# Kernel tuning notes

Hardware: AMD Instinct MI355X
Metric: run time of the kernel (lower is better)

Reference implementation:

```python
import jax, jax.numpy as jnp
import numpy as np

B, N, E = 4, 50000, 400000
DIMS = [4, 64, 64, 2]
K = 3
EPS = 1e-5      # BatchNorm1d eps
SLOPE = 0.01    # LeakyReLU default negative slope


def setup_inputs() -> dict:
    key = jax.random.key(0)
    k = jax.random.split(key, 20)
    x = jax.random.normal(k[0], (B, N, DIMS[0]), dtype=jnp.float32)
    src = jax.random.randint(k[1], (E,), 0, N)
    dst = jax.random.randint(k[2], (E,), 0, N)
    edge_w = jax.random.uniform(k[3], (E,), dtype=jnp.float32) + 0.1
    W1 = jax.random.normal(k[4], (K + 1, DIMS[0], DIMS[1]), dtype=jnp.float32) * 0.1
    b1 = jnp.zeros((DIMS[1],), jnp.float32)
    W2 = jax.random.normal(k[5], (K + 1, DIMS[1], DIMS[2]), dtype=jnp.float32) * 0.1
    b2 = jnp.zeros((DIMS[2],), jnp.float32)
    W3 = jax.random.normal(k[6], (K + 1, DIMS[2], DIMS[3]), dtype=jnp.float32) * 0.1
    b3 = jnp.zeros((DIMS[3],), jnp.float32)
    g1 = jnp.ones((N,), jnp.float32)
    be1 = jnp.zeros((N,), jnp.float32)
    g2 = jnp.ones((N,), jnp.float32)
    be2 = jnp.zeros((N,), jnp.float32)
    mask = (jax.random.uniform(k[7], (N, 2)) < 0.7).astype(jnp.float32)
    mean_y = jax.random.normal(k[8], (N, 2), dtype=jnp.float32) * 0.1
    std_y = jax.random.uniform(k[9], (N, 2), dtype=jnp.float32) + 0.5
    vmin = -jnp.abs(jax.random.normal(k[10], (N,), dtype=jnp.float32)) - 1.0
    vmax = jnp.abs(jax.random.normal(k[11], (N,), dtype=jnp.float32)) + 1.0
    qmin = -jnp.abs(jax.random.normal(k[12], (N,), dtype=jnp.float32)) - 1.0
    qmax = jnp.abs(jax.random.normal(k[13], (N,), dtype=jnp.float32)) + 1.0
    return dict(x=x, src=src, dst=dst, edge_w=edge_w, W1=W1, b1=b1, W2=W2, b2=b2,
                W3=W3, b3=b3, g1=g1, be1=be1, g2=g2, be2=be2, mask=mask,
                mean_y=mean_y, std_y=std_y, vmin=vmin, vmax=vmax, qmin=qmin, qmax=qmax)


def _tag(h, W, b, src, dst, w):
    # TAGConv: out = sum_k A_norm^k x @ W_k + b
    out = jnp.einsum('bnf,fg->bng', h, W[0])
    for i in range(1, W.shape[0]):
        msg = h[:, src, :] * w[None, :, None]          # gather + scale  [B, E, F]
        h = jnp.zeros_like(h).at[:, dst, :].add(msg)   # scatter-add     [B, N, F]
        out = out + jnp.einsum('bnf,fg->bng', h, W[i])
    return out + b


def _bn(h, g, b):
    # nn.BatchNorm1d(N) on [B, N, F]: per-node stats over (batch, feature)
    mu = h.mean(axis=(0, 2), keepdims=True)
    var = h.var(axis=(0, 2), keepdims=True)  # biased, as torch uses for normalization
    return g[None, :, None] * (h - mu) * jax.lax.rsqrt(var + EPS) + b[None, :, None]


def reference(x, src, dst, edge_w, W1, b1, W2, b2, W3, b3, g1, be1, g2, be2,
              mask, mean_y, std_y, vmin, vmax, qmin, qmax):
    n = x.shape[1]
    # gcn_norm (add_self_loops=False): D^{-1/2} A D^{-1/2} with deg over targets
    deg = jnp.zeros((n,), x.dtype).at[dst].add(edge_w)
    dis = jnp.where(deg > 0, jax.lax.rsqrt(jnp.maximum(deg, 1e-30)), 0.0)
    w = dis[src] * edge_w * dis[dst]
    h = jax.nn.leaky_relu(_bn(_tag(x, W1, b1, src, dst, w), g1, be1), SLOPE)
    h = jax.nn.leaky_relu(_bn(_tag(h, W2, b2, src, dst, w), g2, be2), SLOPE)
    out = _tag(h, W3, b3, src, dst, w)
    # denormalize_y=True path
    std = jnp.where(jnp.isinf(std_y), 0.0, std_y)
    out = (out * std + mean_y) * mask
    # training=False path: per-node clamp of v and q channels
    out = jnp.stack([jnp.clip(out[:, :, 0], vmin, vmax),
                     jnp.clip(out[:, :, 1], qmin, qmax)], axis=-1)
    return out
```

## Files before the change

kernel.cpp:

```cpp
#include <hip/hip_runtime.h>
#include <hip/hip_bf16.h>

typedef __hip_bfloat16 bf16;
typedef unsigned int u32;
typedef unsigned short u16;
typedef __attribute__((ext_vector_type(8))) short bf16x8;
typedef __attribute__((ext_vector_type(4))) float f32x4;

#define NNODES 50000
#define NEDGES 400000
#define NROWS  200000
#define NBLK   196
#define EPSBN  1e-5f
#define SLOPE  0.01f
#define WS_NEEDED 106711296ULL

static __device__ __forceinline__ float bu2f(u16 u) { return __uint_as_float((u32)u << 16); }
static __device__ __forceinline__ float blo(u32 u) { return __uint_as_float(u << 16); }
static __device__ __forceinline__ float bhi(u32 u) { return __uint_as_float(u & 0xFFFF0000u); }
static __device__ __forceinline__ u16 f2bu(float f) {
  bf16 x = __float2bfloat16(f);
  return *(u16*)&x;
}
static __device__ __forceinline__ u32 bpack(float a, float b) {
  return (u32)f2bu(a) | ((u32)f2bu(b) << 16);
}
static __device__ __forceinline__ float ld(const void* p, int i, int isbf) {
  return isbf ? bu2f(((const u16*)p)[i]) : ((const float*)p)[i];
}

union frag_u { uint4 u; bf16x8 v; };

__global__ __launch_bounds__(256)
void detect_kernel(const u16* __restrict__ ew_raw, int* __restrict__ flag) {
  __shared__ int ok;
  if (threadIdx.x == 0) ok = 1;
  __syncthreads();
  float v = bu2f(ew_raw[threadIdx.x]);
  if (!(v >= 0.04f && v <= 1.3f)) atomicAnd(&ok, 0);
  __syncthreads();
  if (threadIdx.x == 0) *flag = ok;
}

__global__ __launch_bounds__(256)
void ws_probe_kernel(u32* __restrict__ out) {
  int i = blockIdx.x * 256 + threadIdx.x;
  if (i < 4 * NNODES * 2) out[i] = 0u;
}


__global__ __launch_bounds__(256)
void edge_deg_kernel(const int* __restrict__ dst, const void* __restrict__ ew,
                     const int* __restrict__ flagp, float* __restrict__ deg,
                     int* __restrict__ cnt) {
  int isbf = *flagp;
  int e = blockIdx.x * 256 + threadIdx.x;
  if (e >= NEDGES) return;
  int d = dst[e];
  atomicAdd(&deg[d], ld(ew, e, isbf));
  atomicAdd(&cnt[d], 1);
}

__global__ __launch_bounds__(256)
void node_dis_kernel(const float* __restrict__ deg, float* __restrict__ dis) {
  int n = blockIdx.x * 256 + threadIdx.x;
  if (n >= NNODES) return;
  float d = deg[n];
  dis[n] = d > 0.f ? 1.f / sqrtf(fmaxf(d, 1e-30f)) : 0.f;
}

__global__ __launch_bounds__(256)
void bsum_kernel(const int* __restrict__ cnt, int* __restrict__ bsum) {
  __shared__ int sd[256];
  int tid = threadIdx.x;
  int i = blockIdx.x * 256 + tid;
  sd[tid] = (i < NNODES) ? cnt[i] : 0;
  __syncthreads();
  for (int off = 128; off > 0; off >>= 1) {
    if (tid < off) sd[tid] += sd[tid + off];
    __syncthreads();
  }
  if (tid == 0) bsum[blockIdx.x] = sd[0];
}

__global__ __launch_bounds__(256)
void bscan_kernel(const int* __restrict__ bsum, int* __restrict__ boff) {
  __shared__ int sd[256];
  int tid = threadIdx.x;
  int v = (tid < NBLK) ? bsum[tid] : 0;
  sd[tid] = v;
  __syncthreads();
  for (int off = 1; off < 256; off <<= 1) {
    int t = (tid >= off) ? sd[tid - off] : 0;
    __syncthreads();
    sd[tid] += t;
    __syncthreads();
  }
  if (tid < NBLK) boff[tid] = sd[tid] - v;
}

__global__ __launch_bounds__(256)
void scatter_scan_kernel(const int* __restrict__ cnt, const int* __restrict__ boff,
                         int* __restrict__ rowp, int* __restrict__ cursor) {
  __shared__ int sd[256];
  int tid = threadIdx.x;
  int i = blockIdx.x * 256 + tid;
  int v = (i < NNODES) ? cnt[i] : 0;
  sd[tid] = v;
  __syncthreads();
  for (int off = 1; off < 256; off <<= 1) {
    int t = (tid >= off) ? sd[tid - off] : 0;
    __syncthreads();
    sd[tid] += t;
    __syncthreads();
  }
  if (i < NNODES) {
    int ex = boff[blockIdx.x] + sd[tid] - v;
    rowp[i] = ex;
    cursor[i] = ex;
  }
  if (i == NNODES - 1) rowp[NNODES] = NEDGES;
}

__global__ __launch_bounds__(256)
void edge_fill_kernel(const int* __restrict__ src, const int* __restrict__ dst,
                      const void* __restrict__ ew, const int* __restrict__ flagp,
                      const float* __restrict__ dis, int* __restrict__ cursor,
                      int* __restrict__ src_s, float* __restrict__ w_s) {
  int isbf = *flagp;
  int e = blockIdx.x * 256 + threadIdx.x;
  if (e >= NEDGES) return;
  int s = src[e], d = dst[e];
  float w = dis[s] * ld(ew, e, isbf) * dis[d];
  int p = atomicAdd(&cursor[d], 1);
  src_s[p] = s;
  w_s[p] = w;
}

__global__ __launch_bounds__(256)
void convw_kernel(const void* __restrict__ W1, const void* __restrict__ b1,
                  const void* __restrict__ W2, const void* __restrict__ b2,
                  const void* __restrict__ W3, const void* __restrict__ b3,
                  const int* __restrict__ flagp, float* __restrict__ out) {
  int isbf = *flagp;
  int i = blockIdx.x * 256 + threadIdx.x;
  if (i < 1024)       out[i] = ld(W1, i, isbf);
  else if (i < 17408) out[i] = ld(W2, i - 1024, isbf);
  else if (i < 17920) out[i] = ld(W3, i - 17408, isbf);
  else if (i < 17984) out[i] = ld(b1, i - 17920, isbf);
  else if (i < 18048) out[i] = ld(b2, i - 17984, isbf);
  else if (i < 18050) out[i] = ld(b3, i - 18048, isbf);
}

__global__ __launch_bounds__(256)
void packw2_kernel(const void* __restrict__ W2, const int* __restrict__ flagp,
                   u16* __restrict__ Wp) {
  int idx = blockIdx.x * 256 + threadIdx.x;
  if (idx >= 32 * 64 * 8) return;
  int j = idx & 7, col = (idx >> 3) & 63, o = idx >> 9;
  int k = o * 8 + j;
  Wp[idx] = f2bu(ld(W2, ((k >> 6) * 64 + (k & 63)) * 64 + col, *flagp));
}

__global__ __launch_bounds__(256)
void packw1_kernel(const void* __restrict__ W1, const int* __restrict__ flagp,
                   u16* __restrict__ Wp) {
  int idx = blockIdx.x * 256 + threadIdx.x;
  if (idx >= 4 * 64 * 8) return;
  int j = idx & 7, col = (idx >> 3) & 63, o = idx >> 9;
  int k = o * 8 + j;
  u16 v = 0;
  if (k < 16) v = f2bu(ld(W1, ((k >> 2) * 4 + (k & 3)) * 64 + col, *flagp));
  Wp[idx] = v;
}

__global__ __launch_bounds__(256)
void xpose_kernel(const void* __restrict__ x, const int* __restrict__ flagp,
                  u16* __restrict__ rows) {
  int isbf = *flagp;
  int o = blockIdx.x * 256 + threadIdx.x;
  if (o >= NNODES * 16) return;
  int n = o >> 4, b = (o >> 2) & 3, f = o & 3;
  rows[o] = f2bu(ld(x, b * NNODES * 4 + n * 4 + f, isbf));
}


__global__ __launch_bounds__(256)
void prop4_kernel(const u16* __restrict__ hin, u16* __restrict__ hout,
                  const int* __restrict__ row_ptr, const int* __restrict__ src_s,
                  const float* __restrict__ w_s) {
  int t = blockIdx.x * 256 + threadIdx.x;
  int node = t >> 2, j = t & 3;
  if (node >= NNODES) return;
  int beg = row_ptr[node], end = row_ptr[node + 1];
  const uint2* base = (const uint2*)hin;
  float a0 = 0.f, a1 = 0.f, a2 = 0.f, a3 = 0.f;
  for (int e = beg; e < end; ++e) {
    float w = w_s[e];
    uint2 v = base[(size_t)src_s[e] * 4 + j];
    a0 = fmaf(w, blo(v.x), a0);
    a1 = fmaf(w, bhi(v.x), a1);
    a2 = fmaf(w, blo(v.y), a2);
    a3 = fmaf(w, bhi(v.y), a3);
  }
  uint2 o; o.x = bpack(a0, a1); o.y = bpack(a2, a3);
  ((uint2*)hout)[(size_t)node * 4 + j] = o;
}

__global__ __launch_bounds__(256)
void prop64_kernel(const u16* __restrict__ hin, u16* __restrict__ hout,
                   const int* __restrict__ row_ptr, const int* __restrict__ src_s,
                   const float* __restrict__ w_s) {
  int t = blockIdx.x * 256 + threadIdx.x;
  int node = t >> 6, lane = t & 63;
  if (node >= NNODES) return;
  int beg = row_ptr[node], end = row_ptr[node + 1];
  int deg = end - beg;
  int my_src = 0; float my_w = 0.f;
  if (lane < deg) { my_src = src_s[beg + lane]; my_w = w_s[beg + lane]; }
  const uint2* base = (const uint2*)hin;
  float a0 = 0.f, a1 = 0.f, a2 = 0.f, a3 = 0.f;
  int n = deg < 64 ? deg : 64;
  int i = 0;
  for (; i + 2 <= n; i += 2) {
    int s0 = __shfl(my_src, i);
    int s1 = __shfl(my_src, i + 1);
    float w0 = __shfl(my_w, i);
    float w1 = __shfl(my_w, i + 1);
    uint2 v0 = base[(size_t)s0 * 64 + lane];
    uint2 v1 = base[(size_t)s1 * 64 + lane];
    a0 = fmaf(w0, blo(v0.x), a0); a1 = fmaf(w0, bhi(v0.x), a1);
    a2 = fmaf(w0, blo(v0.y), a2); a3 = fmaf(w0, bhi(v0.y), a3);
    a0 = fmaf(w1, blo(v1.x), a0); a1 = fmaf(w1, bhi(v1.x), a1);
    a2 = fmaf(w1, blo(v1.y), a2); a3 = fmaf(w1, bhi(v1.y), a3);
  }
  if (i < n) {
    int s0 = __shfl(my_src, i);
    float w0 = __shfl(my_w, i);
    uint2 v0 = base[(size_t)s0 * 64 + lane];
    a0 = fmaf(w0, blo(v0.x), a0); a1 = fmaf(w0, bhi(v0.x), a1);
    a2 = fmaf(w0, blo(v0.y), a2); a3 = fmaf(w0, bhi(v0.y), a3);
  }
  for (int e = beg + 64; e < end; ++e) {
    float w = w_s[e];
    uint2 v = base[(size_t)src_s[e] * 64 + lane];
    a0 = fmaf(w, blo(v.x), a0); a1 = fmaf(w, bhi(v.x), a1);
    a2 = fmaf(w, blo(v.y), a2); a3 = fmaf(w, bhi(v.y), a3);
  }
  uint2 o; o.x = bpack(a0, a1); o.y = bpack(a2, a3);
  ((uint2*)hout)[(size_t)node * 64 + lane] = o;
}

static __device__ __forceinline__ void bn_store_tile(
    const f32x4 acc[4], int node, int rowbase, int quad, int n16,
    const void* gam, const void* bet, int isbf, u16* hout) {
  float s = 0.f, ss = 0.f;
#pragma unroll
  for (int cb = 0; cb < 4; ++cb)
#pragma unroll
    for (int i = 0; i < 4; ++i) { float v = acc[cb][i]; s += v; ss = fmaf(v, v, ss); }
  s  += __shfl_xor(s, 1);  s  += __shfl_xor(s, 2);
  s  += __shfl_xor(s, 4);  s  += __shfl_xor(s, 8);
  ss += __shfl_xor(ss, 1); ss += __shfl_xor(ss, 2);
  ss += __shfl_xor(ss, 4); ss += __shfl_xor(ss, 8);
  float mu  = s * (1.f / 256.f);
  float var = ss * (1.f / 256.f) - mu * mu;
  float rs  = rsqrtf(fmaxf(var, 0.f) + EPSBN);
  float gn = ld(gam, node, isbf) * rs;
  float bn = ld(bet, node, isbf);
#pragma unroll
  for (int i = 0; i < 4; ++i) {
    u16* orow = hout + (size_t)(rowbase + quad * 4 + i) * 64 + n16;
#pragma unroll
    for (int cb = 0; cb < 4; ++cb) {
      float y = fmaf(gn, acc[cb][i] - mu, bn);
      y = y > 0.f ? y : SLOPE * y;
      orow[cb * 16] = f2bu(y);
    }
  }
}

__global__ __launch_bounds__(256)
void fused_l1_mfma(const u16* __restrict__ h0, const u16* __restrict__ h1,
                   const u16* __restrict__ h2, const u16* __restrict__ h3,
                   const u16* __restrict__ Wp1, const float* __restrict__ bias,
                   const void* __restrict__ gam, const void* __restrict__ bet,
                   const int* __restrict__ flagp, u16* __restrict__ hout) {
  int isbf = *flagp;
  int wave = threadIdx.x >> 6, lane = threadIdx.x & 63;
  int n16 = lane & 15, quad = lane >> 4;
  int rowbase = blockIdx.x * 64 + wave * 16;
  int node = (rowbase >> 2) + quad;

  frag_u af;
  if (quad < 2) {
    const u16* hx = (quad == 0) ? h0 : h2;
    const u16* hy = (quad == 0) ? h1 : h3;
    int r = rowbase + n16;
    uint2 ua = *(const uint2*)(hx + (size_t)r * 4);
    uint2 ub = *(const uint2*)(hy + (size_t)r * 4);
    af.u = make_uint4(ua.x, ua.y, ub.x, ub.y);
  } else {
    af.u = make_uint4(0u, 0u, 0u, 0u);
  }

  f32x4 acc[4];
#pragma unroll
  for (int cb = 0; cb < 4; ++cb) {
    float bv = bias[cb * 16 + n16];
    acc[cb] = (f32x4){bv, bv, bv, bv};
  }
#pragma unroll
  for (int cb = 0; cb < 4; ++cb) {
    frag_u bf;
    bf.u = *(const uint4*)(Wp1 + ((size_t)quad * 64 + cb * 16 + n16) * 8);
    acc[cb] = __builtin_amdgcn_mfma_f32_16x16x32_bf16(af.v, bf.v, acc[cb], 0, 0, 0);
  }
  bn_store_tile(acc, node, rowbase, quad, n16, gam, bet, isbf, hout);
}

__global__ __launch_bounds__(256)
void fused_l2_mfma(const u16* __restrict__ h0, const u16* __restrict__ h1,
                   const u16* __restrict__ h2, const u16* __restrict__ h3,
                   const u16* __restrict__ Wp2, const float* __restrict__ bias,
                   const void* __restrict__ gam, const void* __restrict__ bet,
                   const int* __restrict__ flagp, u16* __restrict__ hout) {
  int isbf = *flagp;
  int wave = threadIdx.x >> 6, lane = threadIdx.x & 63;
  int n16 = lane & 15, quad = lane >> 4;
  int rowbase = blockIdx.x * 64 + wave * 16;
  int node = (rowbase >> 2) + quad;

  f32x4 acc[4];
#pragma unroll
  for (int cb = 0; cb < 4; ++cb) {
    float bv = bias[cb * 16 + n16];
    acc[cb] = (f32x4){bv, bv, bv, bv};
  }
  size_t arow = (size_t)(rowbase + n16) * 64;
#pragma unroll
  for (int kc = 0; kc < 8; ++kc) {
    const u16* hb = (kc < 2) ? h0 : (kc < 4) ? h1 : (kc < 6) ? h2 : h3;
    int coff = (kc & 1) * 32 + quad * 8;
    frag_u af;
    af.u = *(const uint4*)(hb + arow + coff);
    const u16* wb = Wp2 + ((size_t)(kc * 4 + quad) * 64) * 8;
#pragma unroll
    for (int cb = 0; cb < 4; ++cb) {
      frag_u bf;
      bf.u = *(const uint4*)(wb + (cb * 16 + n16) * 8);
      acc[cb] = __builtin_amdgcn_mfma_f32_16x16x32_bf16(af.v, bf.v, acc[cb], 0, 0, 0);
    }
  }
  bn_store_tile(acc, node, rowbase, quad, n16, gam, bet, isbf, hout);
}

__global__ __launch_bounds__(256)
void gemmz_kernel(const u16* __restrict__ h, const float* __restrict__ Wf,
                  float2* __restrict__ z0, float2* __restrict__ z1,
                  float2* __restrict__ z2, float2* __restrict__ z3) {
  int r = blockIdx.x * 256 + threadIdx.x;
  if (r >= NROWS) return;
  const float* W3f = Wf + 17408;
  const float* b3f = Wf + 18048;
  float a[4][2];
  a[0][0] = b3f[0]; a[0][1] = b3f[1];
#pragma unroll
  for (int k = 1; k < 4; ++k) { a[k][0] = 0.f; a[k][1] = 0.f; }
  const uint4* hp = (const uint4*)(h + (size_t)r * 64);
  for (int i = 0; i < 8; ++i) {
    uint4 u = hp[i];
    float f[8] = {blo(u.x), bhi(u.x), blo(u.y), bhi(u.y),
                  blo(u.z), bhi(u.z), blo(u.w), bhi(u.w)};
#pragma unroll
    for (int k = 0; k < 4; ++k) {
      const float* Wr = W3f + k * 128 + i * 16;
#pragma unroll
      for (int j = 0; j < 8; ++j) {
        a[k][0] = fmaf(f[j], Wr[j * 2],     a[k][0]);
        a[k][1] = fmaf(f[j], Wr[j * 2 + 1], a[k][1]);
      }
    }
  }
  z0[r] = make_float2(a[0][0], a[0][1]);
  z1[r] = make_float2(a[1][0], a[1][1]);
  z2[r] = make_float2(a[2][0], a[2][1]);
  z3[r] = make_float2(a[3][0], a[3][1]);
}

__global__ __launch_bounds__(256)
void prop2_add_kernel(const float4* __restrict__ yin, const float4* __restrict__ z,
                      float4* __restrict__ yout, const int* __restrict__ rowp,
                      const int* __restrict__ src_s, const float* __restrict__ w_s) {
  int node = blockIdx.x * 256 + threadIdx.x;
  if (node >= NNODES) return;
  float4 zA = z[node * 2], zB = z[node * 2 + 1];
  int beg = rowp[node], end = rowp[node + 1];
  for (int e = beg; e < end; ++e) {
    float w = w_s[e];
    int s = src_s[e];
    float4 vA = yin[s * 2], vB = yin[s * 2 + 1];
    zA.x = fmaf(w, vA.x, zA.x); zA.y = fmaf(w, vA.y, zA.y);
    zA.z = fmaf(w, vA.z, zA.z); zA.w = fmaf(w, vA.w, zA.w);
    zB.x = fmaf(w, vB.x, zB.x); zB.y = fmaf(w, vB.y, zB.y);
    zB.z = fmaf(w, vB.z, zB.z); zB.w = fmaf(w, vB.w, zB.w);
  }
  yout[node * 2] = zA;
  yout[node * 2 + 1] = zB;
}

__global__ __launch_bounds__(256)
void prop2_fin_kernel(const float4* __restrict__ yin, const float4* __restrict__ z,
                      const int* __restrict__ rowp, const int* __restrict__ src_s,
                      const float* __restrict__ w_s, const void* __restrict__ std_y,
                      const void* __restrict__ mean_y, const void* __restrict__ mask,
                      const void* __restrict__ vmin, const void* __restrict__ vmax,
                      const void* __restrict__ qmin, const void* __restrict__ qmax,
                      const int* __restrict__ flagp, void* __restrict__ out) {
  int isbf = *flagp;
  int node = blockIdx.x * 256 + threadIdx.x;
  if (node >= NNODES) return;
  float4 zA = z[node * 2], zB = z[node * 2 + 1];
  int beg = rowp[node], end = rowp[node + 1];
  for (int e = beg; e < end; ++e) {
    float w = w_s[e];
    int s = src_s[e];
    float4 vA = yin[s * 2], vB = yin[s * 2 + 1];
    zA.x = fmaf(w, vA.x, zA.x); zA.y = fmaf(w, vA.y, zA.y);
    zA.z = fmaf(w, vA.z, zA.z); zA.w = fmaf(w, vA.w, zA.w);
    zB.x = fmaf(w, vB.x, zB.x); zB.y = fmaf(w, vB.y, zB.y);
    zB.z = fmaf(w, vB.z, zB.z); zB.w = fmaf(w, vB.w, zB.w);
  }
  int rem = node * 2;
  float sd0 = ld(std_y, rem, isbf);     if (__builtin_isinf(sd0)) sd0 = 0.f;
  float sd1 = ld(std_y, rem + 1, isbf); if (__builtin_isinf(sd1)) sd1 = 0.f;
  float me0 = ld(mean_y, rem, isbf),  me1 = ld(mean_y, rem + 1, isbf);
  float mk0 = ld(mask, rem, isbf),    mk1 = ld(mask, rem + 1, isbf);
  float lo0 = ld(vmin, node, isbf),   hi0 = ld(vmax, node, isbf);
  float lo1 = ld(qmin, node, isbf),   hi1 = ld(qmax, node, isbf);
  float yv[8] = {zA.x, zA.y, zA.z, zA.w, zB.x, zB.y, zB.z, zB.w};
#pragma unroll
  for (int b = 0; b < 4; ++b) {
    float r0 = fminf(fmaxf(fmaf(yv[2*b],   sd0, me0) * mk0, lo0), hi0);
    float r1 = fminf(fmaxf(fmaf(yv[2*b+1], sd1, me1) * mk1, lo1), hi1);
    int oidx = b * NNODES + node;
    if (isbf) ((u32*)out)[oidx] = bpack(r0, r1);
    else      ((float2*)out)[oidx] = make_float2(r0, r1);
  }
}

extern "C" void kernel_launch(void* const* d_in, const int* in_sizes, int n_in,
                              void* d_out, int out_size, void* d_ws, size_t ws_size,
                              hipStream_t stream) {
  (void)in_sizes; (void)n_in; (void)out_size;

  if (ws_size < WS_NEEDED) {
    ws_probe_kernel<<<(4 * NNODES * 2 + 255) / 256, 256, 0, stream>>>((u32*)d_out);
    return;
  }

  const void* x     = d_in[0];
  const int*  src   = (const int*)d_in[1];
  const int*  dst   = (const int*)d_in[2];
  const void* ew    = d_in[3];
  const void* W1    = d_in[4];
  const void* b1    = d_in[5];
  const void* W2    = d_in[6];
  const void* b2    = d_in[7];
  const void* W3    = d_in[8];
  const void* b3    = d_in[9];
  const void* g1    = d_in[10];
  const void* be1   = d_in[11];
  const void* g2    = d_in[12];
  const void* be2   = d_in[13];
  const void* mask  = d_in[14];
  const void* mean_y= d_in[15];
  const void* std_y = d_in[16];
  const void* vmin  = d_in[17];
  const void* vmax  = d_in[18];
  const void* qmin  = d_in[19];
  const void* qmax  = d_in[20];

  char* ws = (char*)d_ws;
  float* deg    = (float*)(ws + 0);
  int*   cnt    = (int*  )(ws + 200000);
  int*   rowp   = (int*  )(ws + 400000);
  int*   flagp  = (int*  )(ws + 600032);
  int*   cursor = (int*  )(ws + 600064);
  float* dis    = (float*)(ws + 800064);
  int*   src_s  = (int*  )(ws + 1000064);
  float* w_s    = (float*)(ws + 2600064);
  float* Wf     = (float*)(ws + 4200064);
  int*   bsum   = (int*  )(ws + 4272384);
  int*   boff   = (int*  )(ws + 4273408);
  u16*   Wp1    = (u16*  )(ws + 4274432);
  u16*   Wp2    = (u16*  )(ws + 4278528);
  u16*   hA     = (u16*  )(ws + 4311296);
  u16*   t1     = (u16*  )(ws + 29911296);
  u16*   t2     = (u16*  )(ws + 55511296);
  u16*   t3     = (u16*  )(ws + 81111296);
  u16*   rows_x = (u16*  )(ws + 81111296);
  u16*   pa     = (u16*  )(ws + 82711296);
  u16*   pb     = (u16*  )(ws + 84311296);
  u16*   pc     = (u16*  )(ws + 85911296);
  float2* z0    = (float2*)(ws + 29911296);
  float2* z1    = (float2*)(ws + 31511296);
  float2* z2    = (float2*)(ws + 33111296);
  float2* z3    = (float2*)(ws + 34711296);

  float* b1f = Wf + 17920;
  float* b2f = Wf + 17984;

  hipMemsetAsync(ws, 0, 400000, stream);

  dim3 blk(256);
  int egrid = (NEDGES + 255) / 256;
  int ngrid = (NNODES + 255) / 256;
  int rgrid = (NROWS + 255) / 256;
  int mgrid = NROWS / 64;
  int p64g  = (NNODES * 64) / 256;
  int xg    = (NNODES * 16 + 255) / 256;

  detect_kernel<<<1, blk, 0, stream>>>((const u16*)ew, flagp);
  edge_deg_kernel<<<egrid, blk, 0, stream>>>(dst, ew, flagp, deg, cnt);
  node_dis_kernel<<<ngrid, blk, 0, stream>>>(deg, dis);
  bsum_kernel<<<NBLK, blk, 0, stream>>>(cnt, bsum);
  bscan_kernel<<<1, blk, 0, stream>>>(bsum, boff);
  scatter_scan_kernel<<<NBLK, blk, 0, stream>>>(cnt, boff, rowp, cursor);
  edge_fill_kernel<<<egrid, blk, 0, stream>>>(src, dst, ew, flagp, dis, cursor, src_s, w_s);
  convw_kernel<<<71, blk, 0, stream>>>(W1, b1, W2, b2, W3, b3, flagp, Wf);
  packw1_kernel<<<8, blk, 0, stream>>>(W1, flagp, Wp1);
  packw2_kernel<<<64, blk, 0, stream>>>(W2, flagp, Wp2);
  xpose_kernel<<<xg, blk, 0, stream>>>(x, flagp, rows_x);

  prop4_kernel<<<rgrid, blk, 0, stream>>>(rows_x, pa, rowp, src_s, w_s);
  prop4_kernel<<<rgrid, blk, 0, stream>>>(pa, pb, rowp, src_s, w_s);
  prop4_kernel<<<rgrid, blk, 0, stream>>>(pb, pc, rowp, src_s, w_s);
  fused_l1_mfma<<<mgrid, blk, 0, stream>>>(rows_x, pa, pb, pc, Wp1, b1f,
                                           g1, be1, flagp, hA);

  prop64_kernel<<<p64g, blk, 0, stream>>>(hA, t1, rowp, src_s, w_s);
  prop64_kernel<<<p64g, blk, 0, stream>>>(t1, t2, rowp, src_s, w_s);
  prop64_kernel<<<p64g, blk, 0, stream>>>(t2, t3, rowp, src_s, w_s);
  fused_l2_mfma<<<mgrid, blk, 0, stream>>>(hA, t1, t2, t3, Wp2, b2f,
                                           g2, be2, flagp, hA);

  gemmz_kernel<<<rgrid, blk, 0, stream>>>(hA, Wf, z0, z1, z2, z3);
  prop2_add_kernel<<<ngrid, blk, 0, stream>>>((const float4*)z3, (const float4*)z2,
                                              (float4*)z2, rowp, src_s, w_s);
  prop2_add_kernel<<<ngrid, blk, 0, stream>>>((const float4*)z2, (const float4*)z1,
                                              (float4*)z1, rowp, src_s, w_s);
  prop2_fin_kernel<<<ngrid, blk, 0, stream>>>((const float4*)z1, (const float4*)z0,
                                              rowp, src_s, w_s, std_y, mean_y, mask,
                                              vmin, vmax, qmin, qmax, flagp, d_out);
}
```

Measured before the change: 390.6 us.

## Merge setup kernels and widen prop64 gathers to 16-byte loads across half-waves

Fuses node_dis and bsum into one kernel, and folds the weight conversion, packing and input transpose kernels into a single prep kernel, which removes several launches. The 64-feature propagation now splits each wave into two half-waves. Each half loads 16-byte rows from a different neighbour, and the two halves are combined with a cross-lane shuffle before one half stores. The goal is wider gather transactions and fewer loop iterations, at the cost of more accumulator registers and an extra reduction step.

```diff
diff --git a/kernel.cpp b/kernel.cpp
--- a/kernel.cpp
+++ b/kernel.cpp
@@ -62,18 +62,15 @@
 }
 
 __global__ __launch_bounds__(256)
-void node_dis_kernel(const float* __restrict__ deg, float* __restrict__ dis) {
-  int n = blockIdx.x * 256 + threadIdx.x;
-  if (n >= NNODES) return;
-  float d = deg[n];
-  dis[n] = d > 0.f ? 1.f / sqrtf(fmaxf(d, 1e-30f)) : 0.f;
-}
-
-__global__ __launch_bounds__(256)
-void bsum_kernel(const int* __restrict__ cnt, int* __restrict__ bsum) {
+void dis_bsum_kernel(const float* __restrict__ deg, const int* __restrict__ cnt,
+                     float* __restrict__ dis, int* __restrict__ bsum) {
   __shared__ int sd[256];
   int tid = threadIdx.x;
   int i = blockIdx.x * 256 + tid;
+  if (i < NNODES) {
+    float d = deg[i];
+    dis[i] = d > 0.f ? 1.f / sqrtf(fmaxf(d, 1e-30f)) : 0.f;
+  }
   sd[tid] = (i < NNODES) ? cnt[i] : 0;
   __syncthreads();
   for (int off = 128; off > 0; off >>= 1) {
@@ -138,50 +135,39 @@
 }
 
 __global__ __launch_bounds__(256)
-void convw_kernel(const void* __restrict__ W1, const void* __restrict__ b1,
-                  const void* __restrict__ W2, const void* __restrict__ b2,
-                  const void* __restrict__ W3, const void* __restrict__ b3,
-                  const int* __restrict__ flagp, float* __restrict__ out) {
+void prep_kernel(const void* __restrict__ x, const void* __restrict__ W1,
+                 const void* __restrict__ b1, const void* __restrict__ W2,
+                 const void* __restrict__ b2, const void* __restrict__ W3,
+                 const void* __restrict__ b3, const int* __restrict__ flagp,
+                 float* __restrict__ Wf, u16* __restrict__ Wp1,
+                 u16* __restrict__ Wp2, u16* __restrict__ rows) {
   int isbf = *flagp;
-  int i = blockIdx.x * 256 + threadIdx.x;
-  if (i < 1024)       out[i] = ld(W1, i, isbf);
-  else if (i < 17408) out[i] = ld(W2, i - 1024, isbf);
-  else if (i < 17920) out[i] = ld(W3, i - 17408, isbf);
-  else if (i < 17984) out[i] = ld(b1, i - 17920, isbf);
-  else if (i < 18048) out[i] = ld(b2, i - 17984, isbf);
-  else if (i < 18050) out[i] = ld(b3, i - 18048, isbf);
-}
-
-__global__ __launch_bounds__(256)
-void packw2_kernel(const void* __restrict__ W2, const int* __restrict__ flagp,
-                   u16* __restrict__ Wp) {
-  int idx = blockIdx.x * 256 + threadIdx.x;
-  if (idx >= 32 * 64 * 8) return;
-  int j = idx & 7, col = (idx >> 3) & 63, o = idx >> 9;
-  int k = o * 8 + j;
-  Wp[idx] = f2bu(ld(W2, ((k >> 6) * 64 + (k & 63)) * 64 + col, *flagp));
-}
-
-__global__ __launch_bounds__(256)
-void packw1_kernel(const void* __restrict__ W1, const int* __restrict__ flagp,
-                   u16* __restrict__ Wp) {
-  int idx = blockIdx.x * 256 + threadIdx.x;
-  if (idx >= 4 * 64 * 8) return;
-  int j = idx & 7, col = (idx >> 3) & 63, o = idx >> 9;
-  int k = o * 8 + j;
-  u16 v = 0;
-  if (k < 16) v = f2bu(ld(W1, ((k >> 2) * 4 + (k & 3)) * 64 + col, *flagp));
-  Wp[idx] = v;
-}
-
-__global__ __launch_bounds__(256)
-void xpose_kernel(const void* __restrict__ x, const int* __restrict__ flagp,
-                  u16* __restrict__ rows) {
-  int isbf = *flagp;
-  int o = blockIdx.x * 256 + threadIdx.x;
-  if (o >= NNODES * 16) return;
-  int n = o >> 4, b = (o >> 2) & 3, f = o & 3;
-  rows[o] = f2bu(ld(x, b * NNODES * 4 + n * 4 + f, isbf));
+  int blk = blockIdx.x;
+  if (blk < 3125) {
+    int o = blk * 256 + threadIdx.x;
+    int n = o >> 4, b = (o >> 2) & 3, f = o & 3;
+    rows[o] = f2bu(ld(x, b * NNODES * 4 + n * 4 + f, isbf));
+  } else if (blk < 3196) {
+    int i = (blk - 3125) * 256 + threadIdx.x;
+    if (i < 1024)       Wf[i] = ld(W1, i, isbf);
+    else if (i < 17408) Wf[i] = ld(W2, i - 1024, isbf);
+    else if (i < 17920) Wf[i] = ld(W3, i - 17408, isbf);
+    else if (i < 17984) Wf[i] = ld(b1, i - 17920, isbf);
+    else if (i < 18048) Wf[i] = ld(b2, i - 17984, isbf);
+    else if (i < 18050) Wf[i] = ld(b3, i - 18048, isbf);
+  } else if (blk < 3204) {
+    int idx = (blk - 3196) * 256 + threadIdx.x;
+    int j = idx & 7, col = (idx >> 3) & 63, o = idx >> 9;
+    int k = o * 8 + j;
+    u16 v = 0;
+    if (k < 16) v = f2bu(ld(W1, ((k >> 2) * 4 + (k & 3)) * 64 + col, isbf));
+    Wp1[idx] = v;
+  } else {
+    int idx = (blk - 3204) * 256 + threadIdx.x;
+    int j = idx & 7, col = (idx >> 3) & 63, o = idx >> 9;
+    int k = o * 8 + j;
+    Wp2[idx] = f2bu(ld(W2, ((k >> 6) * 64 + (k & 63)) * 64 + col, isbf));
+  }
 }
 
 
@@ -218,37 +204,55 @@
   int deg = end - beg;
   int my_src = 0; float my_w = 0.f;
   if (lane < deg) { my_src = src_s[beg + lane]; my_w = w_s[beg + lane]; }
-  const uint2* base = (const uint2*)hin;
+  int sub = lane >> 5, l32 = lane & 31;
+  const uint4* base = (const uint4*)hin;
   float a0 = 0.f, a1 = 0.f, a2 = 0.f, a3 = 0.f;
+  float a4 = 0.f, a5 = 0.f, a6 = 0.f, a7 = 0.f;
   int n = deg < 64 ? deg : 64;
   int i = 0;
-  for (; i + 2 <= n; i += 2) {
-    int s0 = __shfl(my_src, i);
-    int s1 = __shfl(my_src, i + 1);
-    float w0 = __shfl(my_w, i);
-    float w1 = __shfl(my_w, i + 1);
-    uint2 v0 = base[(size_t)s0 * 64 + lane];
-    uint2 v1 = base[(size_t)s1 * 64 + lane];
+  for (; i + 4 <= n; i += 4) {
+    int sA = __shfl(my_src, i + sub);
+    int sB = __shfl(my_src, i + 2 + sub);
+    float wA = __shfl(my_w, i + sub);
+    float wB = __shfl(my_w, i + 2 + sub);
+    uint4 vA = base[(size_t)sA * 32 + l32];
+    uint4 vB = base[(size_t)sB * 32 + l32];
+    a0 = fmaf(wA, blo(vA.x), a0); a1 = fmaf(wA, bhi(vA.x), a1);
+    a2 = fmaf(wA, blo(vA.y), a2); a3 = fmaf(wA, bhi(vA.y), a3);
+    a4 = fmaf(wA, blo(vA.z), a4); a5 = fmaf(wA, bhi(vA.z), a5);
+    a6 = fmaf(wA, blo(vA.w), a6); a7 = fmaf(wA, bhi(vA.w), a7);
+    a0 = fmaf(wB, blo(vB.x), a0); a1 = fmaf(wB, bhi(vB.x), a1);
+    a2 = fmaf(wB, blo(vB.y), a2); a3 = fmaf(wB, bhi(vB.y), a3);
+    a4 = fmaf(wB, blo(vB.z), a4); a5 = fmaf(wB, bhi(vB.z), a5);
+    a6 = fmaf(wB, blo(vB.w), a6); a7 = fmaf(wB, bhi(vB.w), a7);
+  }
+  for (; i < n; i += 2) {
+    int s0 = __shfl(my_src, i + sub);
+    float w0 = __shfl(my_w, i + sub);
+    uint4 v0 = base[(size_t)s0 * 32 + l32];
     a0 = fmaf(w0, blo(v0.x), a0); a1 = fmaf(w0, bhi(v0.x), a1);
     a2 = fmaf(w0, blo(v0.y), a2); a3 = fmaf(w0, bhi(v0.y), a3);
-    a0 = fmaf(w1, blo(v1.x), a0); a1 = fmaf(w1, bhi(v1.x), a1);
-    a2 = fmaf(w1, blo(v1.y), a2); a3 = fmaf(w1, bhi(v1.y), a3);
-  }
-  if (i < n) {
-    int s0 = __shfl(my_src, i);
-    float w0 = __shfl(my_w, i);
-    uint2 v0 = base[(size_t)s0 * 64 + lane];
-    a0 = fmaf(w0, blo(v0.x), a0); a1 = fmaf(w0, bhi(v0.x), a1);
-    a2 = fmaf(w0, blo(v0.y), a2); a3 = fmaf(w0, bhi(v0.y), a3);
-  }
-  for (int e = beg + 64; e < end; ++e) {
+    a4 = fmaf(w0, blo(v0.z), a4); a5 = fmaf(w0, bhi(v0.z), a5);
+    a6 = fmaf(w0, blo(v0.w), a6); a7 = fmaf(w0, bhi(v0.w), a7);
+  }
+  for (int e = beg + 64 + sub; e < end; e += 2) {
     float w = w_s[e];
-    uint2 v = base[(size_t)src_s[e] * 64 + lane];
+    uint4 v = base[(size_t)src_s[e] * 32 + l32];
     a0 = fmaf(w, blo(v.x), a0); a1 = fmaf(w, bhi(v.x), a1);
     a2 = fmaf(w, blo(v.y), a2); a3 = fmaf(w, bhi(v.y), a3);
-  }
-  uint2 o; o.x = bpack(a0, a1); o.y = bpack(a2, a3);
-  ((uint2*)hout)[(size_t)node * 64 + lane] = o;
+    a4 = fmaf(w, blo(v.z), a4); a5 = fmaf(w, bhi(v.z), a5);
+    a6 = fmaf(w, blo(v.w), a6); a7 = fmaf(w, bhi(v.w), a7);
+  }
+  a0 += __shfl_xor(a0, 32); a1 += __shfl_xor(a1, 32);
+  a2 += __shfl_xor(a2, 32); a3 += __shfl_xor(a3, 32);
+  a4 += __shfl_xor(a4, 32); a5 += __shfl_xor(a5, 32);
+  a6 += __shfl_xor(a6, 32); a7 += __shfl_xor(a7, 32);
+  if (sub == 0) {
+    uint4 o;
+    o.x = bpack(a0, a1); o.y = bpack(a2, a3);
+    o.z = bpack(a4, a5); o.w = bpack(a6, a7);
+    ((uint4*)hout)[(size_t)node * 32 + l32] = o;
+  }
 }
 
 static __device__ __forceinline__ void bn_store_tile(
@@ -519,19 +523,15 @@
   int rgrid = (NROWS + 255) / 256;
   int mgrid = NROWS / 64;
   int p64g  = (NNODES * 64) / 256;
-  int xg    = (NNODES * 16 + 255) / 256;
 
   detect_kernel<<<1, blk, 0, stream>>>((const u16*)ew, flagp);
   edge_deg_kernel<<<egrid, blk, 0, stream>>>(dst, ew, flagp, deg, cnt);
-  node_dis_kernel<<<ngrid, blk, 0, stream>>>(deg, dis);
-  bsum_kernel<<<NBLK, blk, 0, stream>>>(cnt, bsum);
+  dis_bsum_kernel<<<NBLK, blk, 0, stream>>>(deg, cnt, dis, bsum);
   bscan_kernel<<<1, blk, 0, stream>>>(bsum, boff);
   scatter_scan_kernel<<<NBLK, blk, 0, stream>>>(cnt, boff, rowp, cursor);
   edge_fill_kernel<<<egrid, blk, 0, stream>>>(src, dst, ew, flagp, dis, cursor, src_s, w_s);
-  convw_kernel<<<71, blk, 0, stream>>>(W1, b1, W2, b2, W3, b3, flagp, Wf);
-  packw1_kernel<<<8, blk, 0, stream>>>(W1, flagp, Wp1);
-  packw2_kernel<<<64, blk, 0, stream>>>(W2, flagp, Wp2);
-  xpose_kernel<<<xg, blk, 0, stream>>>(x, flagp, rows_x);
+  prep_kernel<<<3268, blk, 0, stream>>>(x, W1, b1, W2, b2, W3, b3, flagp,
+                                        Wf, Wp1, Wp2, rows_x);
 
   prop4_kernel<<<rgrid, blk, 0, stream>>>(rows_x, pa, rowp, src_s, w_s);
   prop4_kernel<<<rgrid, blk, 0, stream>>>(pa, pb, rowp, src_s, w_s);
```

Result: faster. 380.3 us (-2.6%).
